# Kernel tuning notes

Hardware: AMD Instinct MI355X
Metric: run time of the kernel (lower is better)

## Reference

```python
import jax, jax.numpy as jnp
import numpy as np

B, LQ, LK, D = 32, 2048, 2048, 64


def setup_inputs() -> dict:
    key = jax.random.key(0)
    k1, k2, k3, k4 = jax.random.split(key, 4)
    querys = jax.random.normal(k1, (B, LQ, D), dtype=jnp.float32)
    keys = jax.random.normal(k2, (B, LK, D), dtype=jnp.float32)
    values = jax.random.normal(k3, (B, LK, D), dtype=jnp.float32)
    # valid lengths in [1, LK]
    valid_lens = jax.random.randint(k4, (B,), 1, LK + 1, dtype=jnp.int32)
    return {"querys": querys, "keys": keys, "values": values, "valid_lens": valid_lens}


def reference(querys, keys, values, valid_lens):
    d = querys.shape[-1]
    # [B, Lq, Lk] score matrix
    scores = jnp.einsum("bqd,bkd->bqk", querys, keys) / jnp.sqrt(jnp.asarray(d, querys.dtype))
    # masked softmax: key positions >= valid_len get -1e6 (as in d2l masked_softmax)
    key_pos = jnp.arange(scores.shape[-1], dtype=jnp.int32)  # [Lk]
    mask = key_pos[None, None, :] < valid_lens[:, None, None]  # [B, 1, Lk]
    scores = jnp.where(mask, scores, jnp.asarray(-1e6, scores.dtype))
    attn = jax.nn.softmax(scores, axis=-1)
    # dropout p=0.0 -> identity
    return jnp.einsum("bqk,bkd->bqd", attn, values)
```

## Files before the change

### kernel.cpp

```cpp
#include <hip/hip_runtime.h>
#include <hip/hip_bf16.h>
#include <math.h>


#define B_    32
#define LQ_   2048
#define LK_   2048
#define D_    64
#define SLOTF (64 * 64 + 128)

typedef __attribute__((ext_vector_type(8)))  short bf16x8;
typedef __attribute__((ext_vector_type(4)))  float f32x4;
typedef __attribute__((ext_vector_type(16))) float f32x16;

#if defined(__has_builtin) && __has_builtin(__builtin_amdgcn_exp2f)
#define EXP2(x) __builtin_amdgcn_exp2f(x)
#else
#define EXP2(x) exp2f(x)
#endif

static __device__ __forceinline__ unsigned pk_bf16(float a, float b) {
    __hip_bfloat162 h = __float22bfloat162_rn(float2{a, b});
    return *(unsigned*)&h;
}

__global__ __launch_bounds__(128, 2) void fa_stage1(
    const float* __restrict__ Q, const float* __restrict__ K,
    const float* __restrict__ V, const int* __restrict__ vlen,
    float* __restrict__ O, float* __restrict__ ws,
    int nchunks, int chunk_len)
{
    __shared__ __align__(16) short Kl[64 * 64];
    __shared__ __align__(16) short Vt[64 * 64];

    const int tid  = threadIdx.x;
    const int wave = tid >> 6;
    const int lane = tid & 63;
    const int c31  = lane & 31;
    const int h    = lane >> 5;

    const int qt = blockIdx.x, b = blockIdx.y, cidx = blockIdx.z;
    const int vl = vlen[b];
    const int k_begin = cidx * chunk_len;
    if (k_begin >= vl) return;
    const int k_end = min(k_begin + chunk_len, vl);
    const int nt = (k_end - k_begin + 63) >> 6;
    const int q0 = qt * 64 + wave * 32;
    const int direct = (vl <= chunk_len);

    const float qscale = 0.125f * 1.44269504088896340736f;

    unsigned qfrag[4][4];
#pragma unroll
    for (int ks = 0; ks < 4; ++ks) {
        const float* qp = Q + ((size_t)(b * LQ_ + q0 + c31)) * D_ + ks * 16 + h * 8;
        f32x4 t0 = *(const f32x4*)qp;
        f32x4 t1 = *(const f32x4*)(qp + 4);
#pragma unroll
        for (int jj = 0; jj < 2; ++jj) {
            qfrag[ks][jj]     = pk_bf16(t0[2*jj] * qscale, t0[2*jj+1] * qscale);
            qfrag[ks][jj + 2] = pk_bf16(t1[2*jj] * qscale, t1[2*jj+1] * qscale);
        }
    }

    f32x16 oacc[2];
#pragma unroll
    for (int dt = 0; dt < 2; ++dt)
#pragma unroll
        for (int r = 0; r < 16; ++r) oacc[dt][r] = 0.f;
    float mrun = -INFINITY, lrun = 0.f;

    const int skey = tid >> 1, skh = tid & 1;
    const int vkg  = tid & 7,  vdg = tid >> 3;

    const float* kgp = K + ((size_t)(b * LK_ + k_begin + skey)) * D_ + skh * 32;
    const float* vgp = V + ((size_t)(b * LK_ + k_begin + vkg * 8)) * D_ + vdg * 4;

    f32x4 kr[8], vr[8];
#pragma unroll
    for (int i = 0; i < 8; ++i) kr[i] = *(const f32x4*)(kgp + 4 * i);
#pragma unroll
    for (int i = 0; i < 8; ++i) vr[i] = *(const f32x4*)(vgp + (size_t)i * D_);

    for (int t = 0; t < nt; ++t) {
        const int k0 = k_begin + t * 64;
        if (t) __syncthreads();

        {
            unsigned pk32[16];
#pragma unroll
            for (int m = 0; m < 16; ++m)
                pk32[m] = pk_bf16(kr[m >> 1][2 * (m & 1)], kr[m >> 1][2 * (m & 1) + 1]);
#pragma unroll
            for (int cch = 0; cch < 4; ++cch) {
                const int pos = (skh * 4 + cch) ^ (skey & 7);
                *(bf16x8*)&Kl[skey * 64 + pos * 8] = *(bf16x8*)&pk32[4 * cch];
            }
#pragma unroll
            for (int dr = 0; dr < 4; ++dr) {
                unsigned w[4];
#pragma unroll
                for (int p = 0; p < 4; ++p)
                    w[p] = pk_bf16(vr[2 * p][dr], vr[2 * p + 1][dr]);
                const int dim = vdg * 4 + dr;
                const int pos = vkg ^ (dim & 7);
                *(bf16x8*)&Vt[dim * 64 + pos * 8] = *(bf16x8*)&w[0];
            }
        }
        if (t + 1 < nt) {
            const float* kn = kgp + (size_t)(t + 1) * 64 * D_;
            const float* vn = vgp + (size_t)(t + 1) * 64 * D_;
#pragma unroll
            for (int i = 0; i < 8; ++i) kr[i] = *(const f32x4*)(kn + 4 * i);
#pragma unroll
            for (int i = 0; i < 8; ++i) vr[i] = *(const f32x4*)(vn + (size_t)i * D_);
        }
        __syncthreads();

        f32x16 st[2];
#pragma unroll
        for (int s = 0; s < 2; ++s) {
#pragma unroll
            for (int r = 0; r < 16; ++r) st[s][r] = 0.f;
#pragma unroll
            for (int ks = 0; ks < 4; ++ks) {
                const int pos = (ks * 2 + h) ^ (c31 & 7);
                bf16x8 kf = *(const bf16x8*)&Kl[(s * 32 + c31) * 64 + pos * 8];
                st[s] = __builtin_amdgcn_mfma_f32_32x32x16_bf16(
                    kf, *(const bf16x8*)&qfrag[ks][0], st[s], 0, 0, 0);
            }
        }

        if (k0 + 64 > vl) {
#pragma unroll
            for (int s = 0; s < 2; ++s) {
                const int base = k0 + s * 32 + 4 * h;
#pragma unroll
                for (int r = 0; r < 16; ++r) {
                    const int key = base + (r & 3) + 8 * (r >> 2);
                    if (key >= vl) st[s][r] = -1e30f;
                }
            }
        }

        float mg[8];
#pragma unroll
        for (int s = 0; s < 2; ++s)
#pragma unroll
            for (int g = 0; g < 4; ++g)
                mg[s * 4 + g] = fmaxf(fmaxf(st[s][4*g], st[s][4*g+1]),
                                      fmaxf(st[s][4*g+2], st[s][4*g+3]));
        float tm = fmaxf(fmaxf(fmaxf(mg[0], mg[1]), fmaxf(mg[2], mg[3])),
                         fmaxf(fmaxf(mg[4], mg[5]), fmaxf(mg[6], mg[7])));
        tm = fmaxf(tm, __shfl_xor(tm, 32));
        const float mnew = fmaxf(mrun, tm);
        const float corr = EXP2(mrun - mnew);
        mrun = mnew;
        float rs0 = 0.f, rs1 = 0.f, rs2 = 0.f, rs3 = 0.f;
#pragma unroll
        for (int s = 0; s < 2; ++s)
#pragma unroll
            for (int g = 0; g < 4; ++g) {
                float p0 = EXP2(st[s][4*g]   - mnew);
                float p1 = EXP2(st[s][4*g+1] - mnew);
                float p2 = EXP2(st[s][4*g+2] - mnew);
                float p3 = EXP2(st[s][4*g+3] - mnew);
                st[s][4*g] = p0; st[s][4*g+1] = p1; st[s][4*g+2] = p2; st[s][4*g+3] = p3;
                rs0 += p0; rs1 += p1; rs2 += p2; rs3 += p3;
            }
        float rs = (rs0 + rs1) + (rs2 + rs3);
        rs += __shfl_xor(rs, 32);
        lrun = lrun * corr + rs;
#pragma unroll
        for (int dt = 0; dt < 2; ++dt)
#pragma unroll
            for (int r = 0; r < 16; ++r) oacc[dt][r] *= corr;

        unsigned pk[2][8];
#pragma unroll
        for (int s = 0; s < 2; ++s)
#pragma unroll
            for (int m = 0; m < 8; ++m)
                pk[s][m] = pk_bf16(st[s][2 * m], st[s][2 * m + 1]);

#pragma unroll
        for (int kq = 0; kq < 4; ++kq) {
            const int s = kq >> 1, A4 = (kq & 1) * 4;
            unsigned p0 = pk[s][A4], p1 = pk[s][A4+1], p2 = pk[s][A4+2], p3 = pk[s][A4+3];
            unsigned xp0 = __shfl_xor((int)p0, 32);
            unsigned xp1 = __shfl_xor((int)p1, 32);
            unsigned xp2 = __shfl_xor((int)p2, 32);
            unsigned xp3 = __shfl_xor((int)p3, 32);
            unsigned pf[4];
            pf[0] = h ? xp2 : p0;
            pf[1] = h ? xp3 : p1;
            pf[2] = h ? p2  : xp0;
            pf[3] = h ? p3  : xp1;
            const bf16x8 pfr = *(const bf16x8*)&pf[0];
#pragma unroll
            for (int dt = 0; dt < 2; ++dt) {
                const int pos = (kq * 2 + h) ^ (c31 & 7);
                bf16x8 vf = *(const bf16x8*)&Vt[(dt * 32 + c31) * 64 + pos * 8];
                oacc[dt] = __builtin_amdgcn_mfma_f32_32x32x16_bf16(vf, pfr, oacc[dt], 0, 0, 0);
            }
        }
    }

    if (direct) {
        const float inv = 1.f / lrun;
        float* op = O + ((size_t)(b * LQ_ + q0 + c31)) * D_;
#pragma unroll
        for (int dt = 0; dt < 2; ++dt)
#pragma unroll
            for (int g = 0; g < 4; ++g) {
                f32x4 v;
#pragma unroll
                for (int j = 0; j < 4; ++j) v[j] = oacc[dt][4 * g + j] * inv;
                *(f32x4*)(op + dt * 32 + 8 * g + 4 * h) = v;
            }
    } else {
        float* base = ws + (size_t)((b * 32 + qt) * nchunks + cidx) * SLOTF;
        float* pp = base + (size_t)(wave * 32 + c31) * D_;
#pragma unroll
        for (int dt = 0; dt < 2; ++dt)
#pragma unroll
            for (int g = 0; g < 4; ++g) {
                f32x4 v;
#pragma unroll
                for (int j = 0; j < 4; ++j) v[j] = oacc[dt][4 * g + j];
                *(f32x4*)(pp + dt * 32 + 8 * g + 4 * h) = v;
            }
        if (h == 0) {
            base[64 * 64 + wave * 32 + c31]      = mrun;
            base[64 * 64 + 64 + wave * 32 + c31] = lrun;
        }
    }
}

__global__ __launch_bounds__(256) void fa_combine(
    const float* __restrict__ ws, const int* __restrict__ vlen,
    float* __restrict__ O, int nchunks, int chunk_len)
{
    const int idx = blockIdx.x * 256 + threadIdx.x;
    const int b  = idx >> 15;
    const int vl = vlen[b];
    if (vl <= chunk_len) return;
    const int r  = idx & 32767;
    const int q  = r >> 4;
    const int dg = r & 15;
    const int nc = min(nchunks, (vl + chunk_len - 1) / chunk_len);
    const int qt = q >> 6, ql = q & 63;
    const size_t sbase = (size_t)((b * 32 + qt) * nchunks) * SLOTF;

    float M = -INFINITY;
    for (int c = 0; c < nc; ++c)
        M = fmaxf(M, ws[sbase + (size_t)c * SLOTF + 64 * 64 + ql]);

    f32x4 acc = (f32x4){0.f, 0.f, 0.f, 0.f};
    float L = 0.f;
    for (int c = 0; c < nc; ++c) {
        const float* sb = ws + sbase + (size_t)c * SLOTF;
        const float w = EXP2(sb[64 * 64 + ql] - M);
        L += sb[64 * 64 + 64 + ql] * w;
        f32x4 o4 = *(const f32x4*)(sb + (size_t)ql * D_ + dg * 4);
        acc += o4 * w;
    }
    const float inv = 1.f / L;
    *(f32x4*)(O + (size_t)(b * LQ_ + q) * D_ + dg * 4) = acc * inv;
}

extern "C" void kernel_launch(void* const* d_in, const int* in_sizes, int n_in,
                              void* d_out, int out_size, void* d_ws, size_t ws_size,
                              hipStream_t stream) {
    const float* Q    = (const float*)d_in[0];
    const float* K    = (const float*)d_in[1];
    const float* V    = (const float*)d_in[2];
    const int*   vlen = (const int*)d_in[3];
    float*       O    = (float*)d_out;
    float*       ws   = (float*)d_ws;

    int S = 4;
    while (S > 1 && (size_t)B_ * 32 * S * SLOTF * 4 > ws_size) S >>= 1;
    const int chunk_len = LK_ / S;

    dim3 grid(LQ_ / 64, B_, S);
    fa_stage1<<<grid, dim3(128), 0, stream>>>(Q, K, V, vlen, O, ws, S, chunk_len);
    if (S > 1) {
        const int nthreads = B_ * LQ_ * 16;
        fa_combine<<<dim3(nthreads / 256), dim3(256), 0, stream>>>(ws, vlen, O, S, chunk_len);
    }
}
```

Measured before the change: 177.5 us.

## Schedule attention work items dynamically via global atomic counter

Replaces the static (qtile, batch, chunk) grid mapping with a work-stealing loop where each block fetches item indices from an atomic counter in the workspace. A small kernel resets the counter before each launch. The intent is better load balance across variable valid lengths and cheaper skipping of empty chunks. It adds an extra launch, per-item atomics and barriers.

```diff
diff --git a/kernel.cpp b/kernel.cpp
--- a/kernel.cpp
+++ b/kernel.cpp
@@ -8,6 +8,7 @@
 #define LK_   2048
 #define D_    64
 #define SLOTF (64 * 64 + 128)
+#define WSOFF 64
 
 typedef __attribute__((ext_vector_type(8)))  short bf16x8;
 typedef __attribute__((ext_vector_type(4)))  float f32x4;
@@ -24,14 +25,19 @@
     return *(unsigned*)&h;
 }
 
+__global__ void fa_zero_ctr(int* ctr) {
+    if (threadIdx.x == 0) *ctr = 0;
+}
+
 __global__ __launch_bounds__(128, 2) void fa_stage1(
     const float* __restrict__ Q, const float* __restrict__ K,
     const float* __restrict__ V, const int* __restrict__ vlen,
-    float* __restrict__ O, float* __restrict__ ws,
-    int nchunks, int chunk_len)
+    float* __restrict__ O, float* __restrict__ ws, int* __restrict__ ctr,
+    int nchunks, int chunk_len, int nitems)
 {
     __shared__ __align__(16) short Kl[64 * 64];
     __shared__ __align__(16) short Vt[64 * 64];
+    __shared__ int s_idx;
 
     const int tid  = threadIdx.x;
     const int wave = tid >> 6;
@@ -39,200 +45,211 @@
     const int c31  = lane & 31;
     const int h    = lane >> 5;
 
-    const int qt = blockIdx.x, b = blockIdx.y, cidx = blockIdx.z;
-    const int vl = vlen[b];
-    const int k_begin = cidx * chunk_len;
-    if (k_begin >= vl) return;
-    const int k_end = min(k_begin + chunk_len, vl);
-    const int nt = (k_end - k_begin + 63) >> 6;
-    const int q0 = qt * 64 + wave * 32;
-    const int direct = (vl <= chunk_len);
-
-    const float qscale = 0.125f * 1.44269504088896340736f;
-
-    unsigned qfrag[4][4];
-#pragma unroll
-    for (int ks = 0; ks < 4; ++ks) {
-        const float* qp = Q + ((size_t)(b * LQ_ + q0 + c31)) * D_ + ks * 16 + h * 8;
-        f32x4 t0 = *(const f32x4*)qp;
-        f32x4 t1 = *(const f32x4*)(qp + 4);
-#pragma unroll
-        for (int jj = 0; jj < 2; ++jj) {
-            qfrag[ks][jj]     = pk_bf16(t0[2*jj] * qscale, t0[2*jj+1] * qscale);
-            qfrag[ks][jj + 2] = pk_bf16(t1[2*jj] * qscale, t1[2*jj+1] * qscale);
-        }
-    }
-
-    f32x16 oacc[2];
-#pragma unroll
-    for (int dt = 0; dt < 2; ++dt)
-#pragma unroll
-        for (int r = 0; r < 16; ++r) oacc[dt][r] = 0.f;
-    float mrun = -INFINITY, lrun = 0.f;
-
     const int skey = tid >> 1, skh = tid & 1;
     const int vkg  = tid & 7,  vdg = tid >> 3;
 
-    const float* kgp = K + ((size_t)(b * LK_ + k_begin + skey)) * D_ + skh * 32;
-    const float* vgp = V + ((size_t)(b * LK_ + k_begin + vkg * 8)) * D_ + vdg * 4;
-
-    f32x4 kr[8], vr[8];
-#pragma unroll
-    for (int i = 0; i < 8; ++i) kr[i] = *(const f32x4*)(kgp + 4 * i);
-#pragma unroll
-    for (int i = 0; i < 8; ++i) vr[i] = *(const f32x4*)(vgp + (size_t)i * D_);
-
-    for (int t = 0; t < nt; ++t) {
-        const int k0 = k_begin + t * 64;
-        if (t) __syncthreads();
-
-        {
-            unsigned pk32[16];
-#pragma unroll
-            for (int m = 0; m < 16; ++m)
-                pk32[m] = pk_bf16(kr[m >> 1][2 * (m & 1)], kr[m >> 1][2 * (m & 1) + 1]);
-#pragma unroll
-            for (int cch = 0; cch < 4; ++cch) {
-                const int pos = (skh * 4 + cch) ^ (skey & 7);
-                *(bf16x8*)&Kl[skey * 64 + pos * 8] = *(bf16x8*)&pk32[4 * cch];
-            }
-#pragma unroll
-            for (int dr = 0; dr < 4; ++dr) {
-                unsigned w[4];
-#pragma unroll
-                for (int p = 0; p < 4; ++p)
-                    w[p] = pk_bf16(vr[2 * p][dr], vr[2 * p + 1][dr]);
-                const int dim = vdg * 4 + dr;
-                const int pos = vkg ^ (dim & 7);
-                *(bf16x8*)&Vt[dim * 64 + pos * 8] = *(bf16x8*)&w[0];
+    const float qscale = 0.125f * 1.44269504088896340736f;
+
+    for (;;) {
+        __syncthreads();
+        if (tid == 0) s_idx = atomicAdd(ctr, 1);
+        __syncthreads();
+        const int idx = s_idx;
+        if (idx >= nitems) break;
+
+        const int qt   = idx & 31;
+        const int b    = (idx >> 5) & 31;
+        const int cidx = idx >> 10;
+        const int vl   = vlen[b];
+        const int k_begin = cidx * chunk_len;
+        if (k_begin >= vl) continue;
+
+        const int k_end = min(k_begin + chunk_len, vl);
+        const int nt = (k_end - k_begin + 63) >> 6;
+        const int q0 = qt * 64 + wave * 32;
+        const int direct = (vl <= chunk_len);
+
+        unsigned qfrag[4][4];
+#pragma unroll
+        for (int ks = 0; ks < 4; ++ks) {
+            const float* qp = Q + ((size_t)(b * LQ_ + q0 + c31)) * D_ + ks * 16 + h * 8;
+            f32x4 t0 = *(const f32x4*)qp;
+            f32x4 t1 = *(const f32x4*)(qp + 4);
+#pragma unroll
+            for (int jj = 0; jj < 2; ++jj) {
+                qfrag[ks][jj]     = pk_bf16(t0[2*jj] * qscale, t0[2*jj+1] * qscale);
+                qfrag[ks][jj + 2] = pk_bf16(t1[2*jj] * qscale, t1[2*jj+1] * qscale);
             }
         }
-        if (t + 1 < nt) {
-            const float* kn = kgp + (size_t)(t + 1) * 64 * D_;
-            const float* vn = vgp + (size_t)(t + 1) * 64 * D_;
-#pragma unroll
-            for (int i = 0; i < 8; ++i) kr[i] = *(const f32x4*)(kn + 4 * i);
-#pragma unroll
-            for (int i = 0; i < 8; ++i) vr[i] = *(const f32x4*)(vn + (size_t)i * D_);
+
+        f32x16 oacc[2];
+#pragma unroll
+        for (int dt = 0; dt < 2; ++dt)
+#pragma unroll
+            for (int r = 0; r < 16; ++r) oacc[dt][r] = 0.f;
+        float mrun = -INFINITY, lrun = 0.f;
+
+        const float* kgp = K + ((size_t)(b * LK_ + k_begin + skey)) * D_ + skh * 32;
+        const float* vgp = V + ((size_t)(b * LK_ + k_begin + vkg * 8)) * D_ + vdg * 4;
+
+        f32x4 kr[8], vr[8];
+#pragma unroll
+        for (int i = 0; i < 8; ++i) kr[i] = *(const f32x4*)(kgp + 4 * i);
+#pragma unroll
+        for (int i = 0; i < 8; ++i) vr[i] = *(const f32x4*)(vgp + (size_t)i * D_);
+
+        for (int t = 0; t < nt; ++t) {
+            const int k0 = k_begin + t * 64;
+            if (t) __syncthreads();
+
+            {
+                unsigned pk32[16];
+#pragma unroll
+                for (int m = 0; m < 16; ++m)
+                    pk32[m] = pk_bf16(kr[m >> 1][2 * (m & 1)], kr[m >> 1][2 * (m & 1) + 1]);
+#pragma unroll
+                for (int cch = 0; cch < 4; ++cch) {
+                    const int pos = (skh * 4 + cch) ^ (skey & 7);
+                    *(bf16x8*)&Kl[skey * 64 + pos * 8] = *(bf16x8*)&pk32[4 * cch];
+                }
+#pragma unroll
+                for (int dr = 0; dr < 4; ++dr) {
+                    unsigned w[4];
+#pragma unroll
+                    for (int p = 0; p < 4; ++p)
+                        w[p] = pk_bf16(vr[2 * p][dr], vr[2 * p + 1][dr]);
+                    const int dim = vdg * 4 + dr;
+                    const int pos = vkg ^ (dim & 7);
+                    *(bf16x8*)&Vt[dim * 64 + pos * 8] = *(bf16x8*)&w[0];
+                }
+            }
+            if (t + 1 < nt) {
+                const float* kn = kgp + (size_t)(t + 1) * 64 * D_;
+                const float* vn = vgp + (size_t)(t + 1) * 64 * D_;
+#pragma unroll
+                for (int i = 0; i < 8; ++i) kr[i] = *(const f32x4*)(kn + 4 * i);
+#pragma unroll
+                for (int i = 0; i < 8; ++i) vr[i] = *(const f32x4*)(vn + (size_t)i * D_);
+            }
+            __syncthreads();
+
+            f32x16 st[2];
+#pragma unroll
+            for (int s = 0; s < 2; ++s) {
+#pragma unroll
+                for (int r = 0; r < 16; ++r) st[s][r] = 0.f;
+#pragma unroll
+                for (int ks = 0; ks < 4; ++ks) {
+                    const int pos = (ks * 2 + h) ^ (c31 & 7);
+                    bf16x8 kf = *(const bf16x8*)&Kl[(s * 32 + c31) * 64 + pos * 8];
+                    st[s] = __builtin_amdgcn_mfma_f32_32x32x16_bf16(
+                        kf, *(const bf16x8*)&qfrag[ks][0], st[s], 0, 0, 0);
+                }
+            }
+
+            if (k0 + 64 > vl) {
+#pragma unroll
+                for (int s = 0; s < 2; ++s) {
+                    const int base = k0 + s * 32 + 4 * h;
+#pragma unroll
+                    for (int r = 0; r < 16; ++r) {
+                        const int key = base + (r & 3) + 8 * (r >> 2);
+                        if (key >= vl) st[s][r] = -1e30f;
+                    }
+                }
+            }
+
+            float mg[8];
+#pragma unroll
+            for (int s = 0; s < 2; ++s)
+#pragma unroll
+                for (int g = 0; g < 4; ++g)
+                    mg[s * 4 + g] = fmaxf(fmaxf(st[s][4*g], st[s][4*g+1]),
+                                          fmaxf(st[s][4*g+2], st[s][4*g+3]));
+            float tm = fmaxf(fmaxf(fmaxf(mg[0], mg[1]), fmaxf(mg[2], mg[3])),
+                             fmaxf(fmaxf(mg[4], mg[5]), fmaxf(mg[6], mg[7])));
+            tm = fmaxf(tm, __shfl_xor(tm, 32));
+            const float mnew = fmaxf(mrun, tm);
+            const float corr = EXP2(mrun - mnew);
+            mrun = mnew;
+            float rs0 = 0.f, rs1 = 0.f, rs2 = 0.f, rs3 = 0.f;
+#pragma unroll
+            for (int s = 0; s < 2; ++s)
+#pragma unroll
+                for (int g = 0; g < 4; ++g) {
+                    float p0 = EXP2(st[s][4*g]   - mnew);
+                    float p1 = EXP2(st[s][4*g+1] - mnew);
+                    float p2 = EXP2(st[s][4*g+2] - mnew);
+                    float p3 = EXP2(st[s][4*g+3] - mnew);
+                    st[s][4*g] = p0; st[s][4*g+1] = p1; st[s][4*g+2] = p2; st[s][4*g+3] = p3;
+                    rs0 += p0; rs1 += p1; rs2 += p2; rs3 += p3;
+                }
+            float rs = (rs0 + rs1) + (rs2 + rs3);
+            rs += __shfl_xor(rs, 32);
+            lrun = lrun * corr + rs;
+#pragma unroll
+            for (int dt = 0; dt < 2; ++dt)
+#pragma unroll
+                for (int r = 0; r < 16; ++r) oacc[dt][r] *= corr;
+
+            unsigned pk[2][8];
+#pragma unroll
+            for (int s = 0; s < 2; ++s)
+#pragma unroll
+                for (int m = 0; m < 8; ++m)
+                    pk[s][m] = pk_bf16(st[s][2 * m], st[s][2 * m + 1]);
+
+#pragma unroll
+            for (int kq = 0; kq < 4; ++kq) {
+                const int s = kq >> 1, A4 = (kq & 1) * 4;
+                unsigned p0 = pk[s][A4], p1 = pk[s][A4+1], p2 = pk[s][A4+2], p3 = pk[s][A4+3];
+                unsigned xp0 = __shfl_xor((int)p0, 32);
+                unsigned xp1 = __shfl_xor((int)p1, 32);
+                unsigned xp2 = __shfl_xor((int)p2, 32);
+                unsigned xp3 = __shfl_xor((int)p3, 32);
+                unsigned pf[4];
+                pf[0] = h ? xp2 : p0;
+                pf[1] = h ? xp3 : p1;
+                pf[2] = h ? p2  : xp0;
+                pf[3] = h ? p3  : xp1;
+                const bf16x8 pfr = *(const bf16x8*)&pf[0];
+#pragma unroll
+                for (int dt = 0; dt < 2; ++dt) {
+                    const int pos = (kq * 2 + h) ^ (c31 & 7);
+                    bf16x8 vf = *(const bf16x8*)&Vt[(dt * 32 + c31) * 64 + pos * 8];
+                    oacc[dt] = __builtin_amdgcn_mfma_f32_32x32x16_bf16(vf, pfr, oacc[dt], 0, 0, 0);
+                }
+            }
         }
-        __syncthreads();
-
-        f32x16 st[2];
-#pragma unroll
-        for (int s = 0; s < 2; ++s) {
-#pragma unroll
-            for (int r = 0; r < 16; ++r) st[s][r] = 0.f;
-#pragma unroll
-            for (int ks = 0; ks < 4; ++ks) {
-                const int pos = (ks * 2 + h) ^ (c31 & 7);
-                bf16x8 kf = *(const bf16x8*)&Kl[(s * 32 + c31) * 64 + pos * 8];
-                st[s] = __builtin_amdgcn_mfma_f32_32x32x16_bf16(
-                    kf, *(const bf16x8*)&qfrag[ks][0], st[s], 0, 0, 0);
-            }
-        }
-
-        if (k0 + 64 > vl) {
-#pragma unroll
-            for (int s = 0; s < 2; ++s) {
-                const int base = k0 + s * 32 + 4 * h;
-#pragma unroll
-                for (int r = 0; r < 16; ++r) {
-                    const int key = base + (r & 3) + 8 * (r >> 2);
-                    if (key >= vl) st[s][r] = -1e30f;
-                }
-            }
-        }
-
-        float mg[8];
-#pragma unroll
-        for (int s = 0; s < 2; ++s)
-#pragma unroll
-            for (int g = 0; g < 4; ++g)
-                mg[s * 4 + g] = fmaxf(fmaxf(st[s][4*g], st[s][4*g+1]),
-                                      fmaxf(st[s][4*g+2], st[s][4*g+3]));
-        float tm = fmaxf(fmaxf(fmaxf(mg[0], mg[1]), fmaxf(mg[2], mg[3])),
-                         fmaxf(fmaxf(mg[4], mg[5]), fmaxf(mg[6], mg[7])));
-        tm = fmaxf(tm, __shfl_xor(tm, 32));
-        const float mnew = fmaxf(mrun, tm);
-        const float corr = EXP2(mrun - mnew);
-        mrun = mnew;
-        float rs0 = 0.f, rs1 = 0.f, rs2 = 0.f, rs3 = 0.f;
-#pragma unroll
-        for (int s = 0; s < 2; ++s)
-#pragma unroll
-            for (int g = 0; g < 4; ++g) {
-                float p0 = EXP2(st[s][4*g]   - mnew);
-                float p1 = EXP2(st[s][4*g+1] - mnew);
-                float p2 = EXP2(st[s][4*g+2] - mnew);
-                float p3 = EXP2(st[s][4*g+3] - mnew);
-                st[s][4*g] = p0; st[s][4*g+1] = p1; st[s][4*g+2] = p2; st[s][4*g+3] = p3;
-                rs0 += p0; rs1 += p1; rs2 += p2; rs3 += p3;
-            }
-        float rs = (rs0 + rs1) + (rs2 + rs3);
-        rs += __shfl_xor(rs, 32);
-        lrun = lrun * corr + rs;
-#pragma unroll
-        for (int dt = 0; dt < 2; ++dt)
-#pragma unroll
-            for (int r = 0; r < 16; ++r) oacc[dt][r] *= corr;
-
-        unsigned pk[2][8];
-#pragma unroll
-        for (int s = 0; s < 2; ++s)
-#pragma unroll
-            for (int m = 0; m < 8; ++m)
-                pk[s][m] = pk_bf16(st[s][2 * m], st[s][2 * m + 1]);
-
-#pragma unroll
-        for (int kq = 0; kq < 4; ++kq) {
-            const int s = kq >> 1, A4 = (kq & 1) * 4;
-            unsigned p0 = pk[s][A4], p1 = pk[s][A4+1], p2 = pk[s][A4+2], p3 = pk[s][A4+3];
-            unsigned xp0 = __shfl_xor((int)p0, 32);
-            unsigned xp1 = __shfl_xor((int)p1, 32);
-            unsigned xp2 = __shfl_xor((int)p2, 32);
-            unsigned xp3 = __shfl_xor((int)p3, 32);
-            unsigned pf[4];
-            pf[0] = h ? xp2 : p0;
-            pf[1] = h ? xp3 : p1;
-            pf[2] = h ? p2  : xp0;
-            pf[3] = h ? p3  : xp1;
-            const bf16x8 pfr = *(const bf16x8*)&pf[0];
-#pragma unroll
-            for (int dt = 0; dt < 2; ++dt) {
-                const int pos = (kq * 2 + h) ^ (c31 & 7);
-                bf16x8 vf = *(const bf16x8*)&Vt[(dt * 32 + c31) * 64 + pos * 8];
-                oacc[dt] = __builtin_amdgcn_mfma_f32_32x32x16_bf16(vf, pfr, oacc[dt], 0, 0, 0);
-            }
-        }
-    }
-
-    if (direct) {
-        const float inv = 1.f / lrun;
-        float* op = O + ((size_t)(b * LQ_ + q0 + c31)) * D_;
-#pragma unroll
-        for (int dt = 0; dt < 2; ++dt)
-#pragma unroll
-            for (int g = 0; g < 4; ++g) {
-                f32x4 v;
-#pragma unroll
-                for (int j = 0; j < 4; ++j) v[j] = oacc[dt][4 * g + j] * inv;
-                *(f32x4*)(op + dt * 32 + 8 * g + 4 * h) = v;
-            }
-    } else {
-        float* base = ws + (size_t)((b * 32 + qt) * nchunks + cidx) * SLOTF;
-        float* pp = base + (size_t)(wave * 32 + c31) * D_;
-#pragma unroll
-        for (int dt = 0; dt < 2; ++dt)
-#pragma unroll
-            for (int g = 0; g < 4; ++g) {
-                f32x4 v;
-#pragma unroll
-                for (int j = 0; j < 4; ++j) v[j] = oacc[dt][4 * g + j];
-                *(f32x4*)(pp + dt * 32 + 8 * g + 4 * h) = v;
-            }
-        if (h == 0) {
-            base[64 * 64 + wave * 32 + c31]      = mrun;
-            base[64 * 64 + 64 + wave * 32 + c31] = lrun;
+
+        if (direct) {
+            const float inv = 1.f / lrun;
+            float* op = O + ((size_t)(b * LQ_ + q0 + c31)) * D_;
+#pragma unroll
+            for (int dt = 0; dt < 2; ++dt)
+#pragma unroll
+                for (int g = 0; g < 4; ++g) {
+                    f32x4 v;
+#pragma unroll
+                    for (int j = 0; j < 4; ++j) v[j] = oacc[dt][4 * g + j] * inv;
+                    *(f32x4*)(op + dt * 32 + 8 * g + 4 * h) = v;
+                }
+        } else {
+            float* base = ws + (size_t)((b * 32 + qt) * nchunks + cidx) * SLOTF;
+            float* pp = base + (size_t)(wave * 32 + c31) * D_;
+#pragma unroll
+            for (int dt = 0; dt < 2; ++dt)
+#pragma unroll
+                for (int g = 0; g < 4; ++g) {
+                    f32x4 v;
+#pragma unroll
+                    for (int j = 0; j < 4; ++j) v[j] = oacc[dt][4 * g + j];
+                    *(f32x4*)(pp + dt * 32 + 8 * g + 4 * h) = v;
+                }
+            if (h == 0) {
+                base[64 * 64 + wave * 32 + c31]      = mrun;
+                base[64 * 64 + 64 + wave * 32 + c31] = lrun;
+            }
         }
     }
 }
@@ -277,14 +294,17 @@
     const float* V    = (const float*)d_in[2];
     const int*   vlen = (const int*)d_in[3];
     float*       O    = (float*)d_out;
-    float*       ws   = (float*)d_ws;
+    int*         ctr  = (int*)d_ws;
+    float*       ws   = (float*)d_ws + WSOFF;
 
     int S = 4;
-    while (S > 1 && (size_t)B_ * 32 * S * SLOTF * 4 > ws_size) S >>= 1;
+    while (S > 1 && (size_t)(B_ * 32 * S * SLOTF + WSOFF) * 4 > ws_size) S >>= 1;
     const int chunk_len = LK_ / S;
-
-    dim3 grid(LQ_ / 64, B_, S);
-    fa_stage1<<<grid, dim3(128), 0, stream>>>(Q, K, V, vlen, O, ws, S, chunk_len);
+    const int nitems = 32 * B_ * S;
+
+    fa_zero_ctr<<<dim3(1), dim3(64), 0, stream>>>(ctr);
+    fa_stage1<<<dim3(nitems), dim3(128), 0, stream>>>(Q, K, V, vlen, O, ws, ctr,
+                                                      S, chunk_len, nitems);
     if (S > 1) {
         const int nthreads = B_ * LQ_ * 16;
         fa_combine<<<dim3(nthreads / 256), dim3(256), 0, stream>>>(ws, vlen, O, S, chunk_len);
```

New measurement: 228.4 us. 28.7% more time.
